# Kernel tuning notes

Hardware: AMD Instinct MI355X
Metric: run time of the kernel (lower is better)

Reference implementation:

```python
import jax, jax.numpy as jnp
import numpy as np

B, S, D, H = 1, 4096, 1024, 16
HD = D // H  # 64
THETA = 10000.0


def precompute_freqs_cis(dim, end, theta=THETA):
    freqs = 1.0 / theta ** (np.arange(0, dim, 2, dtype=np.float32) / dim)  # [dim//2]
    t = np.arange(end, dtype=np.float32)
    f = np.outer(t, freqs)                       # [end, dim//2]
    f = np.concatenate((f, f), axis=-1)          # [end, dim]
    return jnp.asarray(np.cos(f), jnp.float32), jnp.asarray(np.sin(f), jnp.float32)


def rotate_half(x):
    x1 = x[..., : x.shape[-1] // 2]
    x2 = x[..., x.shape[-1] // 2:]
    return jnp.concatenate((-x2, x1), axis=-1)


def setup_inputs() -> dict:
    key = jax.random.key(0)
    ks = jax.random.split(key, 5)
    x = jax.random.normal(ks[0], (B, S, D), jnp.float32)
    scale = 0.02
    Wq = jax.random.normal(ks[1], (D, H, HD), jnp.float32) * scale
    Wk = jax.random.normal(ks[2], (D, H, HD), jnp.float32) * scale
    Wv = jax.random.normal(ks[3], (D, H, HD), jnp.float32) * scale
    Wo = jax.random.normal(ks[4], (H, HD, D), jnp.float32) * scale
    mask = jnp.tril(jnp.ones((S, S), jnp.bool_))[None, None]  # [1,1,S,S] causal
    return {"x": x, "mask": mask, "Wq": Wq, "Wk": Wk, "Wv": Wv, "Wo": Wo}


def reference(x, mask, Wq, Wk, Wv, Wo):
    # QKV projections: [B,S,D] x [D,H,HD] -> [B,S,H,HD]
    q = jnp.einsum('bsd,dhe->bshe', x, Wq)
    k = jnp.einsum('bsd,dhe->bshe', x, Wk)
    v = jnp.einsum('bsd,dhe->bshe', x, Wv)
    # Rotary position embedding
    cos, sin = precompute_freqs_cis(HD, S)
    cos = cos[None, :, None, :]  # [1,S,1,HD]
    sin = sin[None, :, None, :]
    q = q * cos + rotate_half(q) * sin
    k = k * cos + rotate_half(k) * sin
    # Scaled dot-product attention
    scale = 1.0 / jnp.sqrt(jnp.asarray(HD, jnp.float32))
    scores = jnp.einsum('bqhe,bkhe->bhqk', q * scale, k)  # [B,H,S,S]
    big_neg = jnp.finfo(scores.dtype).min
    scores = jnp.where(mask, scores, big_neg)
    attn = jax.nn.softmax(scores, axis=-1)
    ctx = jnp.einsum('bhqk,bkhe->bqhe', attn, v)  # [B,S,H,HD]
    # Output projection contracting (head, head_dim)
    out = jnp.einsum('bqhe,hed->bqd', ctx, Wo)  # [B,S,D]
    return out
```

## Files before the change

### kernel.cpp

```cpp
#include <hip/hip_runtime.h>
#include <hip/hip_bf16.h>
#include <stdint.h>
#include <stddef.h>

#define S_LEN 4096
#define DMODEL 1024
#define NHEAD 16
#define HDIM 64
#define L2E 1.4426950408889634f
#define FIXED_M 8.0f

typedef __attribute__((ext_vector_type(8))) short bf16x8;
typedef __attribute__((ext_vector_type(8))) unsigned short u16x8;
typedef __attribute__((ext_vector_type(4))) float f32x4;
typedef __attribute__((ext_vector_type(16))) float f32x16;

__device__ __forceinline__ unsigned short f2bf(float f) {
    unsigned int u = __float_as_uint(f);
    return (unsigned short)((u + 0x7FFFu + ((u >> 16) & 1u)) >> 16);
}
__device__ __forceinline__ float bf2f(unsigned short h) {
    return __uint_as_float(((unsigned int)h) << 16);
}

__global__ __launch_bounds__(256) void rope_table_kernel(float* __restrict__ ctab,
                                                         float* __restrict__ stab) {
    int i = blockIdx.x * 256 + threadIdx.x;
    int s = i >> 5, j = i & 31;
    float freq = exp2f(-0.41524101186092407f * (float)j);
    float ang = (float)s * freq;
    ctab[i] = cosf(ang);
    stab[i] = sinf(ang);
}

__global__ __launch_bounds__(256) void cvt_x_kernel(const float* __restrict__ x,
                                                    unsigned short* __restrict__ xb) {
    int i = (blockIdx.x * 256 + threadIdx.x) * 8;
    f32x4 a = *(const f32x4*)(x + i);
    f32x4 b = *(const f32x4*)(x + i + 4);
    u16x8 o;
    #pragma unroll
    for (int j = 0; j < 4; ++j) { o[j] = f2bf(a[j]); o[4 + j] = f2bf(b[j]); }
    *(u16x8*)(xb + i) = o;
}

__global__ __launch_bounds__(256) void cvt_wt_kernel(
    const float* __restrict__ w0, const float* __restrict__ w1,
    const float* __restrict__ w2, const float* __restrict__ w3,
    unsigned short* __restrict__ t0, unsigned short* __restrict__ t1,
    unsigned short* __restrict__ t2, unsigned short* __restrict__ t3) {
    const float* src; unsigned short* dst;
    switch (blockIdx.z) {
        case 0: src = w0; dst = t0; break;
        case 1: src = w1; dst = t1; break;
        case 2: src = w2; dst = t2; break;
        default: src = w3; dst = t3; break;
    }
    __shared__ float tile[64][65];
    int t = threadIdx.x;
    int k0 = blockIdx.y * 64, n0 = blockIdx.x * 64;
    int r = t >> 2, q4 = (t & 3) * 16;
    const float* sp = src + (size_t)(k0 + r) * DMODEL + n0 + q4;
    #pragma unroll
    for (int j = 0; j < 4; ++j) {
        f32x4 v = *(const f32x4*)(sp + j * 4);
        #pragma unroll
        for (int e = 0; e < 4; ++e) tile[r][q4 + j * 4 + e] = v[e];
    }
    __syncthreads();
    int n = t >> 2, kq = (t & 3) * 16;
    unsigned short* dp = dst + (size_t)(n0 + n) * DMODEL + k0 + kq;
    u16x8 a, b;
    #pragma unroll
    for (int j = 0; j < 8; ++j) { a[j] = f2bf(tile[kq + j][n]); b[j] = f2bf(tile[kq + 8 + j][n]); }
    *(u16x8*)dp = a;
    *(u16x8*)(dp + 8) = b;
}

template<int MODE>
__global__ __launch_bounds__(256) void gemm_kernel(
    const unsigned short* __restrict__ Ab,
    const unsigned short* __restrict__ B0,
    const unsigned short* __restrict__ B1,
    const unsigned short* __restrict__ B2,
    unsigned short* __restrict__ o0,
    unsigned short* __restrict__ o1,
    unsigned short* __restrict__ o2,
    float* __restrict__ fo,
    const float* __restrict__ ctab,
    const float* __restrict__ stab) {
    int z = blockIdx.z;
    const unsigned short* Bt = (MODE == 0) ? B0 : (z == 0 ? B0 : (z == 1 ? B1 : B2));
    unsigned short* outp     = (MODE == 0) ? o0 : (z == 0 ? o0 : (z == 1 ? o1 : o2));
    int m0 = blockIdx.y * 128, n0 = blockIdx.x * 128;
    __shared__ unsigned short As[128][72];
    __shared__ unsigned short Bs[128][72];
    int t = threadIdx.x, w = t >> 6, l = t & 63;
    int wm = w >> 1, wn = w & 1, g = l >> 4, c = l & 15;

    f32x4 acc[4][4];
    #pragma unroll
    for (int m = 0; m < 4; ++m)
        #pragma unroll
        for (int n = 0; n < 4; ++n) acc[m][n] = (f32x4){0.f, 0.f, 0.f, 0.f};

    int sr = t >> 1, scc = (t & 1) * 32;

    for (int kt = 0; kt < DMODEL; kt += 64) {
        __syncthreads();
        {
            const unsigned short* gp = Ab + (size_t)(m0 + sr) * DMODEL + kt + scc;
            #pragma unroll
            for (int j = 0; j < 4; ++j)
                *(u16x8*)&As[sr][scc + j * 8] = *(const u16x8*)(gp + j * 8);
        }
        {
            const unsigned short* gp = Bt + (size_t)(n0 + sr) * DMODEL + kt + scc;
            #pragma unroll
            for (int j = 0; j < 4; ++j)
                *(u16x8*)&Bs[sr][scc + j * 8] = *(const u16x8*)(gp + j * 8);
        }
        __syncthreads();
        #pragma unroll
        for (int kk = 0; kk < 64; kk += 32) {
            bf16x8 af[4], bf[4];
            #pragma unroll
            for (int m = 0; m < 4; ++m) af[m] = *(const bf16x8*)&As[wm * 64 + m * 16 + c][kk + g * 8];
            #pragma unroll
            for (int n = 0; n < 4; ++n) bf[n] = *(const bf16x8*)&Bs[wn * 64 + n * 16 + c][kk + g * 8];
            #pragma unroll
            for (int m = 0; m < 4; ++m)
                #pragma unroll
                for (int n = 0; n < 4; ++n)
                    acc[m][n] = __builtin_amdgcn_mfma_f32_16x16x32_bf16(af[m], bf[n], acc[m][n], 0, 0, 0);
        }
    }

    if (MODE == 1 && z < 2) {
        float sc8 = (z == 0) ? 0.125f * L2E : 1.0f;
        #pragma unroll
        for (int m = 0; m < 4; ++m) {
            #pragma unroll
            for (int r = 0; r < 4; ++r) {
                int srow = m0 + wm * 64 + m * 16 + g * 4 + r;
                #pragma unroll
                for (int n = 0; n < 2; ++n) {
                    int e = n * 16 + c;
                    float cs = ctab[srow * 32 + e];
                    float sn = stab[srow * 32 + e];
                    float lo = acc[m][n][r], hi = acc[m][n + 2][r];
                    float nlo = (lo * cs - hi * sn) * sc8;
                    float nhi = (hi * cs + lo * sn) * sc8;
                    size_t base = (size_t)srow * DMODEL + n0 + wn * 64;
                    outp[base + n * 16 + c]       = f2bf(nlo);
                    outp[base + (n + 2) * 16 + c] = f2bf(nhi);
                }
            }
        }
    } else if (MODE == 1) {
        #pragma unroll
        for (int m = 0; m < 4; ++m)
            #pragma unroll
            for (int r = 0; r < 4; ++r) {
                int srow = m0 + wm * 64 + m * 16 + g * 4 + r;
                size_t base = (size_t)srow * DMODEL + n0 + wn * 64;
                #pragma unroll
                for (int n = 0; n < 4; ++n)
                    outp[base + n * 16 + c] = f2bf(acc[m][n][r]);
            }
    } else {
        #pragma unroll
        for (int m = 0; m < 4; ++m)
            #pragma unroll
            for (int r = 0; r < 4; ++r) {
                int srow = m0 + wm * 64 + m * 16 + g * 4 + r;
                size_t base = (size_t)srow * DMODEL + n0 + wn * 64;
                #pragma unroll
                for (int n = 0; n < 4; ++n)
                    fo[base + n * 16 + c] = acc[m][n][r];
            }
    }
}

__global__ __launch_bounds__(512, 4) void attn_kernel(
    const unsigned short* __restrict__ q,
    const unsigned short* __restrict__ k,
    const unsigned short* __restrict__ v,
    unsigned short* __restrict__ ctx,
    unsigned short* __restrict__ Opart,
    float* __restrict__ lpart) {
    int h = blockIdx.x;
    int pair = blockIdx.y;
    int p = blockIdx.z;
    int t = threadIdx.x, w = t >> 6, l = t & 63, c = l & 31, hi = l >> 5;
    int rg = w & 3, ks = w >> 2;

    __shared__ __align__(16) char smraw[36864];
    unsigned short (*KsT)[64][72] = (unsigned short (*)[64][72])smraw;
    unsigned short (*VtT)[64][72] = (unsigned short (*)[64][72])(smraw + 18432);
    float (*Om)[32][64] = (float (*)[32][64])smraw;
    float* ml           = (float*)(smraw + 32768);

    int ts = t & 255;
    int skr = ts >> 2, skc = (ts & 3) * 16;
    int svr = ts & 63, svc = ((ts >> 6) & 3) * 16;
    const unsigned short* gkb = k + (size_t)skr * DMODEL + h * HDIM + skc;
    const unsigned short* gvb = v + (size_t)svr * DMODEL + h * HDIM + svc;

    auto run_segment = [&](int qb, int t0, int cnt, bool finalize) {
        int qrow = qb * 128 + rg * 32 + c;
        int wrmax = qb * 128 + rg * 32 + 31;

        bf16x8 qf[4];
        {
            const unsigned short* qp = q + (size_t)qrow * DMODEL + h * HDIM + hi * 8;
            #pragma unroll
            for (int s = 0; s < 4; ++s) qf[s] = *(const bf16x8*)(qp + s * 16);
        }
        f32x16 o0, o1;
        #pragma unroll
        for (int i = 0; i < 16; ++i) { o0[i] = 0.f; o1[i] = 0.f; }
        float lsum = 0.f;

        u16x8 ka, kb, va, vb;
        if (ks < cnt) {
            size_t off = (size_t)((t0 + ks) * 64) * DMODEL;
            ka = *(const u16x8*)(gkb + off);
            kb = *(const u16x8*)(gkb + off + 8);
            va = *(const u16x8*)(gvb + off);
            vb = *(const u16x8*)(gvb + off + 8);
            *(u16x8*)&KsT[ks][skr][skc]     = ka;
            *(u16x8*)&KsT[ks][skr][skc + 8] = kb;
            #pragma unroll
            for (int j = 0; j < 8; ++j) {
                VtT[ks][svc + j][svr]     = va[j];
                VtT[ks][svc + 8 + j][svr] = vb[j];
            }
        }

        int NIT = (cnt + 1) >> 1;
        for (int it = 0; it < NIT; ++it) {
            int j = 2 * it + ks;
            int kv0 = (t0 + j) * 64;
            if (j + 2 < cnt) {
                size_t off = (size_t)(kv0 + 128) * DMODEL;
                ka = *(const u16x8*)(gkb + off);
                kb = *(const u16x8*)(gkb + off + 8);
                va = *(const u16x8*)(gvb + off);
                vb = *(const u16x8*)(gvb + off + 8);
            }
            __syncthreads();

            if (j < cnt) {
                #pragma unroll
                for (int h2 = 0; h2 < 2; ++h2) {
                    int kbase = kv0 + h2 * 32;
                    if (kbase > wrmax) continue;

                    f32x16 sf;
                    #pragma unroll
                    for (int i = 0; i < 16; ++i) sf[i] = 0.f;
                    __builtin_amdgcn_s_setprio(1);
                    #pragma unroll
                    for (int s = 0; s < 4; ++s) {
                        bf16x8 kf = *(const bf16x8*)&KsT[ks][h2 * 32 + c][s * 16 + hi * 8];
                        sf = __builtin_amdgcn_mfma_f32_32x32x16_bf16(kf, qf[s], sf, 0, 0, 0);
                    }
                    __builtin_amdgcn_s_setprio(0);

                    if (kbase + 31 >= wrmax) {
                        #pragma unroll
                        for (int r = 0; r < 16; ++r) {
                            int key = kbase + (r & 3) + 8 * (r >> 2) + 4 * hi;
                            if (key > qrow) sf[r] = -3.0e38f;
                        }
                    }

                    float ps = 0.f;
                    unsigned int dw[8];
                    #pragma unroll
                    for (int jj = 0; jj < 8; ++jj) {
                        float p0 = exp2f(sf[2 * jj]     - FIXED_M);
                        float p1 = exp2f(sf[2 * jj + 1] - FIXED_M);
                        ps += p0 + p1;
                        union { struct { __hip_bfloat16 x, y; } hh; unsigned int u; } cv;
                        cv.hh.x = __float2bfloat16(p0);
                        cv.hh.y = __float2bfloat16(p1);
                        dw[jj] = cv.u;
                    }
                    lsum += ps;

                    {
                        auto r0 = __builtin_amdgcn_permlane32_swap(dw[0], dw[2], false, false);
                        dw[0] = r0[0]; dw[2] = r0[1];
                        auto r1 = __builtin_amdgcn_permlane32_swap(dw[1], dw[3], false, false);
                        dw[1] = r1[0]; dw[3] = r1[1];
                        auto r2 = __builtin_amdgcn_permlane32_swap(dw[4], dw[6], false, false);
                        dw[4] = r2[0]; dw[6] = r2[1];
                        auto r3 = __builtin_amdgcn_permlane32_swap(dw[5], dw[7], false, false);
                        dw[5] = r3[0]; dw[7] = r3[1];
                    }
                    union { unsigned int u[8]; bf16x8 v[2]; } pu;
                    #pragma unroll
                    for (int jj = 0; jj < 8; ++jj) pu.u[jj] = dw[jj];

                    __builtin_amdgcn_s_setprio(1);
                    {
                        bf16x8 vf00 = *(const bf16x8*)&VtT[ks][c][h2 * 32 + hi * 8];
                        bf16x8 vf01 = *(const bf16x8*)&VtT[ks][c][h2 * 32 + 16 + hi * 8];
                        bf16x8 vf10 = *(const bf16x8*)&VtT[ks][32 + c][h2 * 32 + hi * 8];
                        bf16x8 vf11 = *(const bf16x8*)&VtT[ks][32 + c][h2 * 32 + 16 + hi * 8];
                        o0 = __builtin_amdgcn_mfma_f32_32x32x16_bf16(pu.v[0], vf00, o0, 0, 0, 0);
                        o0 = __builtin_amdgcn_mfma_f32_32x32x16_bf16(pu.v[1], vf01, o0, 0, 0, 0);
                        o1 = __builtin_amdgcn_mfma_f32_32x32x16_bf16(pu.v[0], vf10, o1, 0, 0, 0);
                        o1 = __builtin_amdgcn_mfma_f32_32x32x16_bf16(pu.v[1], vf11, o1, 0, 0, 0);
                    }
                    __builtin_amdgcn_s_setprio(0);
                }
            }

            if (it + 1 < NIT) {
                __syncthreads();
                if (j + 2 < cnt) {
                    *(u16x8*)&KsT[ks][skr][skc]     = ka;
                    *(u16x8*)&KsT[ks][skr][skc + 8] = kb;
                    #pragma unroll
                    for (int jj = 0; jj < 8; ++jj) {
                        VtT[ks][svc + jj][svr]     = va[jj];
                        VtT[ks][svc + 8 + jj][svr] = vb[jj];
                    }
                }
            }
        }

        lsum += __shfl_xor(lsum, 32, 64);

        __syncthreads();
        if (ks == 0) {
            #pragma unroll
            for (int r = 0; r < 16; ++r) {
                int rl = (r & 3) + 8 * (r >> 2) + 4 * hi;
                Om[rg][rl][c]      = o0[r];
                Om[rg][rl][c + 32] = o1[r];
            }
            if (hi == 0) ml[(rg << 5) + c] = lsum;
        }
        __syncthreads();
        if (ks == 1) {
            float lc = ml[(rg << 5) + c] + lsum;
            if (finalize) {
                float inv = 1.0f / lc;
                #pragma unroll
                for (int r = 0; r < 16; ++r) {
                    int rl = (r & 3) + 8 * (r >> 2) + 4 * hi;
                    float invr = __shfl(inv, rl, 32);
                    int grow = qb * 128 + rg * 32 + rl;
                    size_t cb = (size_t)grow * DMODEL + h * HDIM + c;
                    ctx[cb]      = f2bf((Om[rg][rl][c]      + o0[r]) * invr);
                    ctx[cb + 32] = f2bf((Om[rg][rl][c + 32] + o1[r]) * invr);
                }
            } else {
                #pragma unroll
                for (int r = 0; r < 16; ++r) {
                    int rl = (r & 3) + 8 * (r >> 2) + 4 * hi;
                    int grow = qb * 128 + rg * 32 + rl;
                    size_t ob = ((size_t)(p * 16 + h) * 4096 + grow) * 64 + c;
                    Opart[ob]      = f2bf(Om[rg][rl][c]      + o0[r]);
                    Opart[ob + 32] = f2bf(Om[rg][rl][c + 32] + o1[r]);
                }
                if (hi == 0)
                    lpart[(size_t)(p * 16 + h) * 4096 + qrow] = lc;
            }
        }
        __syncthreads();
    };

    if (p == 0) {
        run_segment(pair, 0, 2 * pair + 2, true);
        run_segment(31 - pair, 0, 31 - 2 * pair, false);
    } else {
        run_segment(31 - pair, 31 - 2 * pair, 33, false);
    }
}

__global__ __launch_bounds__(256) void attn_merge_kernel(
    const unsigned short* __restrict__ Op,
    const float* __restrict__ lp,
    unsigned short* __restrict__ ctx) {
    int i = blockIdx.x * 256 + threadIdx.x;
    int g8 = i & 7;
    int row = 2048 + ((i >> 3) & 2047);
    int h = i >> 14;
    size_t idx = (size_t)h * 4096 + row;
    const size_t PS = (size_t)16 * 4096;
    float inv = 1.0f / (lp[idx] + lp[PS + idx]);
    u16x8 v0 = *(const u16x8*)(Op + idx * 64 + g8 * 8);
    u16x8 v1 = *(const u16x8*)(Op + (PS + idx) * 64 + g8 * 8);
    u16x8 o;
    #pragma unroll
    for (int j = 0; j < 8; ++j)
        o[j] = f2bf((bf2f(v0[j]) + bf2f(v1[j])) * inv);
    *(u16x8*)(ctx + (size_t)row * DMODEL + h * 64 + g8 * 8) = o;
}

extern "C" void kernel_launch(void* const* d_in, const int* in_sizes, int n_in,
                              void* d_out, int out_size, void* d_ws, size_t ws_size,
                              hipStream_t stream) {
    const float* x  = (const float*)d_in[0];
    const float* Wq = (const float*)d_in[2];
    const float* Wk = (const float*)d_in[3];
    const float* Wv = (const float*)d_in[4];
    const float* Wo = (const float*)d_in[5];

    char* ws = (char*)d_ws;
    float* ctab = (float*)(ws);
    float* stab = (float*)(ws + (512u << 10));
    unsigned short* ctx = (unsigned short*)(ws + (1u  << 20));
    unsigned short* Wtq = (unsigned short*)(ws + (1u  << 20));
    unsigned short* Wtk = (unsigned short*)(ws + (3u  << 20));
    unsigned short* Wtv = (unsigned short*)(ws + (5u  << 20));
    unsigned short* Wto = (unsigned short*)(ws + (9u  << 20));
    unsigned short* kr  = (unsigned short*)(ws + (11u << 20));
    unsigned short* vb  = (unsigned short*)(ws + (19u << 20));
    unsigned short* qr  = (unsigned short*)(ws + (27u << 20));
    unsigned short* xb  = (unsigned short*)(ws + (35u << 20));
    unsigned short* Opart = (unsigned short*)(ws + (43u << 20));
    float* lpart = (float*)(ws + (59u << 20));

    rope_table_kernel<<<(S_LEN * 32) / 256, 256, 0, stream>>>(ctab, stab);
    cvt_x_kernel<<<(S_LEN * DMODEL) / 2048, 256, 0, stream>>>(x, xb);
    cvt_wt_kernel<<<dim3(16, 16, 4), 256, 0, stream>>>(Wq, Wk, Wv, Wo, Wtq, Wtk, Wtv, Wto);
    gemm_kernel<1><<<dim3(8, 32, 3), 256, 0, stream>>>(xb, Wtq, Wtk, Wtv,
                                                       qr, kr, vb, nullptr, ctab, stab);
    attn_kernel<<<dim3(16, 16, 2), 512, 0, stream>>>(qr, kr, vb, ctx, Opart, lpart);
    attn_merge_kernel<<<(16 * 2048 * 8) / 256, 256, 0, stream>>>(Opart, lpart, ctx);
    gemm_kernel<0><<<dim3(8, 32, 1), 256, 0, stream>>>(ctx, Wto, nullptr, nullptr,
                                                       nullptr, nullptr, nullptr,
                                                       (float*)d_out, ctab, stab);
}
```

Baseline: 163.9 us.

## Split causal attention work into four KV chunks per head pair

```diff
diff --git a/kernel.cpp b/kernel.cpp
--- a/kernel.cpp
+++ b/kernel.cpp
@@ -191,7 +191,7 @@
     float* __restrict__ lpart) {
     int h = blockIdx.x;
     int pair = blockIdx.y;
-    int p = blockIdx.z;
+    int chunk = blockIdx.z;
     int t = threadIdx.x, w = t >> 6, l = t & 63, c = l & 31, hi = l >> 5;
     int rg = w & 3, ks = w >> 2;
 
@@ -207,7 +207,7 @@
     const unsigned short* gkb = k + (size_t)skr * DMODEL + h * HDIM + skc;
     const unsigned short* gvb = v + (size_t)svr * DMODEL + h * HDIM + svc;
 
-    auto run_segment = [&](int qb, int t0, int cnt, bool finalize) {
+    auto run_segment = [&](int qb, int t0, int cnt, bool finalize, int slot) {
         int qrow = qb * 128 + rg * 32 + c;
         int wrmax = qb * 128 + rg * 32 + 31;
 
@@ -364,22 +364,29 @@
                 for (int r = 0; r < 16; ++r) {
                     int rl = (r & 3) + 8 * (r >> 2) + 4 * hi;
                     int grow = qb * 128 + rg * 32 + rl;
-                    size_t ob = ((size_t)(p * 16 + h) * 4096 + grow) * 64 + c;
+                    size_t ob = ((size_t)(slot * 16 + h) * 3072 + (grow - 1024)) * 64 + c;
                     Opart[ob]      = f2bf(Om[rg][rl][c]      + o0[r]);
                     Opart[ob + 32] = f2bf(Om[rg][rl][c + 32] + o1[r]);
                 }
                 if (hi == 0)
-                    lpart[(size_t)(p * 16 + h) * 4096 + qrow] = lc;
+                    lpart[(size_t)(slot * 16 + h) * 3072 + (qrow - 1024)] = lc;
             }
         }
         __syncthreads();
     };
 
-    if (p == 0) {
-        run_segment(pair, 0, 2 * pair + 2, true);
-        run_segment(31 - pair, 0, 31 - 2 * pair, false);
-    } else {
-        run_segment(31 - pair, 31 - 2 * pair, 33, false);
+    int s = (chunk < 2) ? chunk * 17 : 34 + (chunk - 2) * 16;
+    int e = s + ((chunk < 2) ? 17 : 16);
+    int nA = 2 * pair + 2;
+    if (s < nA) {
+        int cntA = ((e < nA) ? e : nA) - s;
+        bool fin = (s == 0 && e >= nA);
+        run_segment(pair, s, cntA, fin, chunk);
+    }
+    if (e > nA) {
+        int bs = ((s > nA) ? s : nA) - nA;
+        int cntB = e - ((s > nA) ? s : nA);
+        run_segment(31 - pair, bs, cntB, false, chunk);
     }
 }
 
@@ -389,17 +396,27 @@
     unsigned short* __restrict__ ctx) {
     int i = blockIdx.x * 256 + threadIdx.x;
     int g8 = i & 7;
-    int row = 2048 + ((i >> 3) & 2047);
-    int h = i >> 14;
-    size_t idx = (size_t)h * 4096 + row;
-    const size_t PS = (size_t)16 * 4096;
-    float inv = 1.0f / (lp[idx] + lp[PS + idx]);
-    u16x8 v0 = *(const u16x8*)(Op + idx * 64 + g8 * 8);
-    u16x8 v1 = *(const u16x8*)(Op + (PS + idx) * 64 + g8 * 8);
+    int r1 = (i >> 3) % 3072;
+    int h = i / (3072 * 8);
+    int row = 1024 + r1;
+    int qb = row >> 7;
+    unsigned mask = (qb < 16) ? 0x3u : (qb < 24 ? 0xEu : 0xFu);
+    const size_t PS = (size_t)16 * 3072;
+    size_t idx = (size_t)h * 3072 + r1;
+    float lsum = 0.f;
+    float acc[8] = {0.f, 0.f, 0.f, 0.f, 0.f, 0.f, 0.f, 0.f};
+    #pragma unroll
+    for (int cs = 0; cs < 4; ++cs) {
+        if (!(mask & (1u << cs))) continue;
+        lsum += lp[cs * PS + idx];
+        u16x8 vv = *(const u16x8*)(Op + (cs * PS + idx) * 64 + g8 * 8);
+        #pragma unroll
+        for (int j = 0; j < 8; ++j) acc[j] += bf2f(vv[j]);
+    }
+    float inv = 1.0f / lsum;
     u16x8 o;
     #pragma unroll
-    for (int j = 0; j < 8; ++j)
-        o[j] = f2bf((bf2f(v0[j]) + bf2f(v1[j])) * inv);
+    for (int j = 0; j < 8; ++j) o[j] = f2bf(acc[j] * inv);
     *(u16x8*)(ctx + (size_t)row * DMODEL + h * 64 + g8 * 8) = o;
 }
 
@@ -424,7 +441,7 @@
     unsigned short* vb  = (unsigned short*)(ws + (19u << 20));
     unsigned short* qr  = (unsigned short*)(ws + (27u << 20));
     unsigned short* xb  = (unsigned short*)(ws + (35u << 20));
-    unsigned short* Opart = (unsigned short*)(ws + (43u << 20));
+    unsigned short* Opart = (unsigned short*)(ws + (35u << 20));
     float* lpart = (float*)(ws + (59u << 20));
 
     rope_table_kernel<<<(S_LEN * 32) / 256, 256, 0, stream>>>(ctab, stab);
@@ -432,8 +449,8 @@
     cvt_wt_kernel<<<dim3(16, 16, 4), 256, 0, stream>>>(Wq, Wk, Wv, Wo, Wtq, Wtk, Wtv, Wto);
     gemm_kernel<1><<<dim3(8, 32, 3), 256, 0, stream>>>(xb, Wtq, Wtk, Wtv,
                                                        qr, kr, vb, nullptr, ctab, stab);
-    attn_kernel<<<dim3(16, 16, 2), 512, 0, stream>>>(qr, kr, vb, ctx, Opart, lpart);
-    attn_merge_kernel<<<(16 * 2048 * 8) / 256, 256, 0, stream>>>(Opart, lpart, ctx);
+    attn_kernel<<<dim3(16, 16, 4), 512, 0, stream>>>(qr, kr, vb, ctx, Opart, lpart);
+    attn_merge_kernel<<<(16 * 3072 * 8) / 256, 256, 0, stream>>>(Opart, lpart, ctx);
     gemm_kernel<0><<<dim3(8, 32, 1), 256, 0, stream>>>(ctx, Wto, nullptr, nullptr,
                                                        nullptr, nullptr, nullptr,
                                                        (float*)d_out, ctab, stab);
```

Result: slower. 167.5 us (+2.2%).

## Swap PV MFMA operand order to drop permlane swaps and vectorize epilogue stores

Applied to the files above, without the earlier changes.

```diff
diff --git a/kernel.cpp b/kernel.cpp
--- a/kernel.cpp
+++ b/kernel.cpp
@@ -198,12 +198,13 @@
     __shared__ __align__(16) char smraw[36864];
     unsigned short (*KsT)[64][72] = (unsigned short (*)[64][72])smraw;
     unsigned short (*VtT)[64][72] = (unsigned short (*)[64][72])(smraw + 18432);
-    float (*Om)[32][64] = (float (*)[32][64])smraw;
-    float* ml           = (float*)(smraw + 32768);
+    float (*Om2)[66] = (float (*)[66])smraw;
+    float* ml2       = (float*)(smraw + 33792);
 
     int ts = t & 255;
     int skr = ts >> 2, skc = (ts & 3) * 16;
     int svr = ts & 63, svc = ((ts >> 6) & 3) * 16;
+    int svp = (svr & ~0xC) | ((svr & 4) << 1) | ((svr & 8) >> 1);
     const unsigned short* gkb = k + (size_t)skr * DMODEL + h * HDIM + skc;
     const unsigned short* gvb = v + (size_t)svr * DMODEL + h * HDIM + svc;
 
@@ -233,8 +234,8 @@
             *(u16x8*)&KsT[ks][skr][skc + 8] = kb;
             #pragma unroll
             for (int j = 0; j < 8; ++j) {
-                VtT[ks][svc + j][svr]     = va[j];
-                VtT[ks][svc + 8 + j][svr] = vb[j];
+                VtT[ks][svc + j][svp]     = va[j];
+                VtT[ks][svc + 8 + j][svp] = vb[j];
             }
         }
 
@@ -277,7 +278,7 @@
                     }
 
                     float ps = 0.f;
-                    unsigned int dw[8];
+                    union { unsigned int u[8]; bf16x8 v[2]; } pu;
                     #pragma unroll
                     for (int jj = 0; jj < 8; ++jj) {
                         float p0 = exp2f(sf[2 * jj]     - FIXED_M);
@@ -286,34 +287,20 @@
                         union { struct { __hip_bfloat16 x, y; } hh; unsigned int u; } cv;
                         cv.hh.x = __float2bfloat16(p0);
                         cv.hh.y = __float2bfloat16(p1);
-                        dw[jj] = cv.u;
+                        pu.u[jj] = cv.u;
                     }
                     lsum += ps;
 
-                    {
-                        auto r0 = __builtin_amdgcn_permlane32_swap(dw[0], dw[2], false, false);
-                        dw[0] = r0[0]; dw[2] = r0[1];
-                        auto r1 = __builtin_amdgcn_permlane32_swap(dw[1], dw[3], false, false);
-                        dw[1] = r1[0]; dw[3] = r1[1];
-                        auto r2 = __builtin_amdgcn_permlane32_swap(dw[4], dw[6], false, false);
-                        dw[4] = r2[0]; dw[6] = r2[1];
-                        auto r3 = __builtin_amdgcn_permlane32_swap(dw[5], dw[7], false, false);
-                        dw[5] = r3[0]; dw[7] = r3[1];
-                    }
-                    union { unsigned int u[8]; bf16x8 v[2]; } pu;
-                    #pragma unroll
-                    for (int jj = 0; jj < 8; ++jj) pu.u[jj] = dw[jj];
-
                     __builtin_amdgcn_s_setprio(1);
                     {
-                        bf16x8 vf00 = *(const bf16x8*)&VtT[ks][c][h2 * 32 + hi * 8];
-                        bf16x8 vf01 = *(const bf16x8*)&VtT[ks][c][h2 * 32 + 16 + hi * 8];
-                        bf16x8 vf10 = *(const bf16x8*)&VtT[ks][32 + c][h2 * 32 + hi * 8];
-                        bf16x8 vf11 = *(const bf16x8*)&VtT[ks][32 + c][h2 * 32 + 16 + hi * 8];
-                        o0 = __builtin_amdgcn_mfma_f32_32x32x16_bf16(pu.v[0], vf00, o0, 0, 0, 0);
-                        o0 = __builtin_amdgcn_mfma_f32_32x32x16_bf16(pu.v[1], vf01, o0, 0, 0, 0);
-                        o1 = __builtin_amdgcn_mfma_f32_32x32x16_bf16(pu.v[0], vf10, o1, 0, 0, 0);
-                        o1 = __builtin_amdgcn_mfma_f32_32x32x16_bf16(pu.v[1], vf11, o1, 0, 0, 0);
+                        bf16x8 a00 = *(const bf16x8*)&VtT[ks][c][h2 * 32 + hi * 8];
+                        bf16x8 a01 = *(const bf16x8*)&VtT[ks][c][h2 * 32 + 16 + hi * 8];
+                        bf16x8 a10 = *(const bf16x8*)&VtT[ks][32 + c][h2 * 32 + hi * 8];
+                        bf16x8 a11 = *(const bf16x8*)&VtT[ks][32 + c][h2 * 32 + 16 + hi * 8];
+                        o0 = __builtin_amdgcn_mfma_f32_32x32x16_bf16(a00, pu.v[0], o0, 0, 0, 0);
+                        o0 = __builtin_amdgcn_mfma_f32_32x32x16_bf16(a01, pu.v[1], o0, 0, 0, 0);
+                        o1 = __builtin_amdgcn_mfma_f32_32x32x16_bf16(a10, pu.v[0], o1, 0, 0, 0);
+                        o1 = __builtin_amdgcn_mfma_f32_32x32x16_bf16(a11, pu.v[1], o1, 0, 0, 0);
                     }
                     __builtin_amdgcn_s_setprio(0);
                 }
@@ -326,8 +313,8 @@
                     *(u16x8*)&KsT[ks][skr][skc + 8] = kb;
                     #pragma unroll
                     for (int jj = 0; jj < 8; ++jj) {
-                        VtT[ks][svc + jj][svr]     = va[jj];
-                        VtT[ks][svc + 8 + jj][svr] = vb[jj];
+                        VtT[ks][svc + jj][svp]     = va[jj];
+                        VtT[ks][svc + 8 + jj][svp] = vb[jj];
                     }
                 }
             }
@@ -339,37 +326,42 @@
         if (ks == 0) {
             #pragma unroll
             for (int r = 0; r < 16; ++r) {
-                int rl = (r & 3) + 8 * (r >> 2) + 4 * hi;
-                Om[rg][rl][c]      = o0[r];
-                Om[rg][rl][c + 32] = o1[r];
-            }
-            if (hi == 0) ml[(rg << 5) + c] = lsum;
+                int dim = (r & 3) + 8 * (r >> 2) + 4 * hi;
+                Om2[rg * 32 + c][dim]      = o0[r];
+                Om2[rg * 32 + c][dim + 32] = o1[r];
+            }
+            if (hi == 0) ml2[rg * 32 + c] = lsum;
         }
         __syncthreads();
         if (ks == 1) {
-            float lc = ml[(rg << 5) + c] + lsum;
+            float lc = ml2[rg * 32 + c] + lsum;
+            float sc = finalize ? 1.0f / lc : 1.0f;
+            #pragma unroll
+            for (int r = 0; r < 16; ++r) {
+                int dim = (r & 3) + 8 * (r >> 2) + 4 * hi;
+                Om2[rg * 32 + c][dim]      = (Om2[rg * 32 + c][dim]      + o0[r]) * sc;
+                Om2[rg * 32 + c][dim + 32] = (Om2[rg * 32 + c][dim + 32] + o1[r]) * sc;
+            }
+            if (!finalize && hi == 0)
+                lpart[(size_t)(p * 16 + h) * 4096 + qrow] = lc;
+        }
+        __syncthreads();
+        {
+            int row = t >> 2, d0 = (t & 3) * 16;
+            u16x8 oa, ob;
+            #pragma unroll
+            for (int j = 0; j < 8; ++j) {
+                oa[j] = f2bf(Om2[row][d0 + j]);
+                ob[j] = f2bf(Om2[row][d0 + 8 + j]);
+            }
             if (finalize) {
-                float inv = 1.0f / lc;
-                #pragma unroll
-                for (int r = 0; r < 16; ++r) {
-                    int rl = (r & 3) + 8 * (r >> 2) + 4 * hi;
-                    float invr = __shfl(inv, rl, 32);
-                    int grow = qb * 128 + rg * 32 + rl;
-                    size_t cb = (size_t)grow * DMODEL + h * HDIM + c;
-                    ctx[cb]      = f2bf((Om[rg][rl][c]      + o0[r]) * invr);
-                    ctx[cb + 32] = f2bf((Om[rg][rl][c + 32] + o1[r]) * invr);
-                }
+                size_t cb = (size_t)(qb * 128 + row) * DMODEL + h * HDIM + d0;
+                *(u16x8*)&ctx[cb]     = oa;
+                *(u16x8*)&ctx[cb + 8] = ob;
             } else {
-                #pragma unroll
-                for (int r = 0; r < 16; ++r) {
-                    int rl = (r & 3) + 8 * (r >> 2) + 4 * hi;
-                    int grow = qb * 128 + rg * 32 + rl;
-                    size_t ob = ((size_t)(p * 16 + h) * 4096 + grow) * 64 + c;
-                    Opart[ob]      = f2bf(Om[rg][rl][c]      + o0[r]);
-                    Opart[ob + 32] = f2bf(Om[rg][rl][c + 32] + o1[r]);
-                }
-                if (hi == 0)
-                    lpart[(size_t)(p * 16 + h) * 4096 + qrow] = lc;
+                size_t obase = ((size_t)(p * 16 + h) * 4096 + qb * 128 + row) * 64 + d0;
+                *(u16x8*)&Opart[obase]     = oa;
+                *(u16x8*)&Opart[obase + 8] = ob;
             }
         }
         __syncthreads();
```

Result: no change. 162.6 us (-0.8%).
